# Kernel tuning notes

Hardware: AMD Instinct MI355X
Metric: run time of the kernel (lower is better)

Reference implementation:

```python
import jax, jax.numpy as jnp
import numpy as np

EMBED_DIM = 1024
NUM_HEADS = 16
HEAD_DIM = EMBED_DIM // NUM_HEADS


def setup_inputs() -> dict:
    key = jax.random.key(0)
    ks = jax.random.split(key, 8)
    B, S, D = 4, 2048, EMBED_DIM
    scale = 1.0 / np.sqrt(D)
    return {
        "values": jax.random.normal(ks[0], (B, S, D), jnp.float32),
        "keys": jax.random.normal(ks[1], (B, S, D), jnp.float32),
        "query": jax.random.normal(ks[2], (B, S, D), jnp.float32),
        "Wv": jax.random.normal(ks[3], (D, D), jnp.float32) * scale,
        "Wk": jax.random.normal(ks[4], (D, D), jnp.float32) * scale,
        "Wq": jax.random.normal(ks[5], (D, D), jnp.float32) * scale,
        "Wo": jax.random.normal(ks[6], (D, D), jnp.float32) * scale,
        "bo": jnp.zeros((D,), jnp.float32),
    }


def reference(values, keys, query, Wv, Wk, Wq, Wo, bo):
    N = query.shape[0]
    H, Dh = NUM_HEADS, HEAD_DIM
    # torch Linear: x @ W.T  (weights stored [out, in])
    v = (values @ Wv.T).reshape(N, -1, H, Dh)
    k = (keys @ Wk.T).reshape(N, -1, H, Dh)
    q = (query @ Wq.T).reshape(N, -1, H, Dh)
    # energy: [N, H, q, k]
    energy = jnp.einsum("nqhd,nkhd->nhqk", q, k)
    # NOTE: original scales by sqrt(embed_dim), not sqrt(head_dim)
    attn = jax.nn.softmax(energy / jnp.sqrt(jnp.float32(EMBED_DIM)), axis=3)
    out = jnp.einsum("nhql,nlhd->nqhd", attn, v).reshape(N, -1, H * Dh)
    return out @ Wo.T + bo
```

## Files before the change

### kernel.cpp

```cpp
#include <hip/hip_runtime.h>
#include <stdint.h>

#define S_LEN   2048
#define D_MODEL 1024
#define N_HEADS 16
#define D_HEAD  64
#define BATCH   4
#define GM      8192
#define GN      1024
#define GK      1024

typedef __attribute__((ext_vector_type(8)))  short short8;
typedef __attribute__((ext_vector_type(4)))  short short4v;
typedef __attribute__((ext_vector_type(4)))  float f32x4;
typedef __attribute__((ext_vector_type(16))) float f32x16;

__device__ __forceinline__ short f2bf(float f) {
  unsigned u = __builtin_bit_cast(unsigned, f);
  u += 0x7fffu + ((u >> 16) & 1u);
  return (short)(u >> 16);
}

__device__ __forceinline__ unsigned cvt_pk_bf16(float lo, float hi) {
  unsigned r;
  asm("v_cvt_pk_bf16_f32 %0, %1, %2" : "=v"(r) : "v"(lo), "v"(hi));
  return r;
}

__device__ __forceinline__ short8 cvtf8(const float4 f0, const float4 f1) {
  unsigned u[4] = { cvt_pk_bf16(f0.x, f0.y), cvt_pk_bf16(f0.z, f0.w),
                    cvt_pk_bf16(f1.x, f1.y), cvt_pk_bf16(f1.z, f1.w) };
  return __builtin_bit_cast(short8, *(ulonglong2*)u);
}

__device__ __forceinline__ void gload_lds16(const short* g, short* lds_base) {
  __builtin_amdgcn_global_load_lds(
      (const __attribute__((address_space(1))) void*)(const void*)g,
      (__attribute__((address_space(3))) void*)(void*)lds_base, 16, 0, 0);
}

__global__ __launch_bounds__(256)
void cast_w(const float* __restrict__ W0, const float* __restrict__ W1,
            const float* __restrict__ W2, const float* __restrict__ W3,
            short* __restrict__ O0, short* __restrict__ O1,
            short* __restrict__ O2, short* __restrict__ O3)
{
  const int y = blockIdx.y;
  const float* src = (y == 0) ? W0 : (y == 1) ? W1 : (y == 2) ? W2 : W3;
  short*       dst = (y == 0) ? O0 : (y == 1) ? O1 : (y == 2) ? O2 : O3;
  const int gid = blockIdx.x * 256 + threadIdx.x;
  const int row = gid >> 7, gr = gid & 127;
  const int og  = (gr & ~7) | ((gr & 7) ^ (row & 7));
  const float* p = src + row * 1024 + gr * 8;
  short8 v = cvtf8(*(const float4*)p, *(const float4*)(p + 4));
  *(short8*)(dst + row * 1024 + og * 8) = v;
}

__global__ __launch_bounds__(256, 3)
void gemm_qkv(const float* __restrict__ Aq, const float* __restrict__ Ak,
              const float* __restrict__ Av,
              const short* __restrict__ Bq, const short* __restrict__ Bk,
              const short* __restrict__ Bv,
              short* __restrict__ Cq, short* __restrict__ Ck,
              short* __restrict__ Cv, float qscale)
{
  __shared__ short As[128 * 64];
  __shared__ short Bs[128 * 64];

  const int p  = blockIdx.x + (blockIdx.y << 3) + (blockIdx.z << 9);
  const int lg = (p & 7) * 192 + (p >> 3);
  const int z  = lg >> 9;
  const int by = (lg >> 3) & 63;
  const int bx = lg & 7;

  const float* Af = (z == 0) ? Aq : (z == 1) ? Ak : Av;
  const short* Bw = (z == 0) ? Bq : (z == 1) ? Bk : Bv;

  const int t = threadIdx.x;
  const int l = t & 63, w = t >> 6;
  const int lo = l & 15, g = l >> 4;
  const int wr = (w >> 1) * 64, wc = (w & 1) * 64;

  const int srow0 = w * 8 + (l >> 3);
  const int sg = l & 7;

  f32x4 acc[4][4] = {};

  for (int kk = 0; kk < GK; kk += 64) {
#pragma unroll
    for (int i = 0; i < 4; ++i) {
      const int row = i * 32 + srow0;
      gload_lds16(Bw + (size_t)(bx * 128 + row) * GK + kk + sg * 8,
                  (short*)((char*)Bs + i * 4096 + w * 1024));
    }
#pragma unroll
    for (int i = 0; i < 4; ++i) {
      const int row = i * 32 + srow0;
      const float* p2 = Af + (size_t)(by * 128 + row) * GK + kk + sg * 8;
      short8 v = cvtf8(*(const float4*)p2, *(const float4*)(p2 + 4));
      *(short8*)(&As[row * 64 + ((sg ^ (row & 7)) * 8)]) = v;
    }
    __syncthreads();

#pragma unroll
    for (int kh = 0; kh < 2; ++kh) {
      short8 a[4], b[4];
      const int gg = ((kh * 4 + g) ^ (lo & 7)) * 8;
#pragma unroll
      for (int mi = 0; mi < 4; ++mi)
        a[mi] = *(const short8*)(&As[(wr + mi * 16 + lo) * 64 + gg]);
#pragma unroll
      for (int ni = 0; ni < 4; ++ni)
        b[ni] = *(const short8*)(&Bs[(wc + ni * 16 + lo) * 64 + gg]);
#pragma unroll
      for (int mi = 0; mi < 4; ++mi)
#pragma unroll
        for (int ni = 0; ni < 4; ++ni)
          acc[mi][ni] = __builtin_amdgcn_mfma_f32_16x16x32_bf16(a[mi], b[ni], acc[mi][ni], 0, 0, 0);
    }
    __syncthreads();
  }

  const int rbase = by * 128 + wr + g * 4;
  const int cbase = bx * 128 + wc + lo;

  if (z < 2) {
    short* C = (z == 0) ? Cq : Ck;
    const float scale = (z == 0) ? qscale : 1.0f;
#pragma unroll
    for (int mi = 0; mi < 4; ++mi)
#pragma unroll
      for (int ni = 0; ni < 4; ++ni)
#pragma unroll
        for (int r = 0; r < 4; ++r)
          C[(size_t)(rbase + mi * 16 + r) * GN + cbase + ni * 16] = f2bf(acc[mi][ni][r] * scale);
  } else {
#pragma unroll
    for (int mi = 0; mi < 4; ++mi)
#pragma unroll
      for (int ni = 0; ni < 4; ++ni) {
        short4v v = {f2bf(acc[mi][ni][0]), f2bf(acc[mi][ni][1]),
                     f2bf(acc[mi][ni][2]), f2bf(acc[mi][ni][3])};
        *(short4v*)(&Cv[(size_t)(cbase + ni * 16) * GM + rbase + mi * 16]) = v;
      }
  }
}

__global__ __launch_bounds__(256, 3)
void gemm_out(const short* __restrict__ Ab, const short* __restrict__ Bw,
              float* __restrict__ C, const float* __restrict__ bias)
{
  __shared__ short As[128 * 64];
  __shared__ short Bs[128 * 64];

  const int p  = blockIdx.x + (blockIdx.y << 3);
  const int lg = (p & 7) * 64 + (p >> 3);
  const int by = lg >> 3;
  const int bx = lg & 7;

  const int t = threadIdx.x;
  const int l = t & 63, w = t >> 6;
  const int lo = l & 15, g = l >> 4;
  const int wr = (w >> 1) * 64, wc = (w & 1) * 64;

  const int srow0 = w * 8 + (l >> 3);
  const int sg = l & 7;

  f32x4 acc[4][4] = {};

  for (int kk = 0; kk < GK; kk += 64) {
#pragma unroll
    for (int i = 0; i < 4; ++i) {
      const int row = i * 32 + srow0;
      gload_lds16(Bw + (size_t)(bx * 128 + row) * GK + kk + sg * 8,
                  (short*)((char*)Bs + i * 4096 + w * 1024));
      gload_lds16(Ab + (size_t)(by * 128 + row) * GK + kk + sg * 8,
                  (short*)((char*)As + i * 4096 + w * 1024));
    }
    __syncthreads();

#pragma unroll
    for (int kh = 0; kh < 2; ++kh) {
      short8 a[4], b[4];
      const int gg = ((kh * 4 + g) ^ (lo & 7)) * 8;
#pragma unroll
      for (int mi = 0; mi < 4; ++mi)
        a[mi] = *(const short8*)(&As[(wr + mi * 16 + lo) * 64 + gg]);
#pragma unroll
      for (int ni = 0; ni < 4; ++ni)
        b[ni] = *(const short8*)(&Bs[(wc + ni * 16 + lo) * 64 + gg]);
#pragma unroll
      for (int mi = 0; mi < 4; ++mi)
#pragma unroll
        for (int ni = 0; ni < 4; ++ni)
          acc[mi][ni] = __builtin_amdgcn_mfma_f32_16x16x32_bf16(a[mi], b[ni], acc[mi][ni], 0, 0, 0);
    }
    __syncthreads();
  }

  const int rbase = by * 128 + wr + g * 4;
  const int cbase = bx * 128 + wc + lo;
#pragma unroll
  for (int ni = 0; ni < 4; ++ni) {
    const float bs = bias[cbase + ni * 16];
#pragma unroll
    for (int mi = 0; mi < 4; ++mi)
#pragma unroll
      for (int r = 0; r < 4; ++r)
        C[(size_t)(rbase + mi * 16 + r) * GN + cbase + ni * 16] = acc[mi][ni][r] + bs;
  }
}

__global__ __launch_bounds__(256, 3)
void attn_fwd4(const short* __restrict__ Q, const short* __restrict__ Kp,
               const short* __restrict__ Vt, short* __restrict__ O)
{
  __shared__ __align__(16) char smem[32768];

  const int bid = blockIdx.x;
  const int ol = ((bid & 7) << 7) | (bid >> 3);
  const int qt = ol & 15, h = (ol >> 4) & 15, n = ol >> 8;

  const int t = threadIdx.x, w = t >> 6, l = t & 63;
  const int lq = l & 31, hi = l >> 5;

  const short* qp = Q + ((size_t)(n * S_LEN + qt * 128 + w * 32 + lq)) * D_MODEL
                      + h * D_HEAD + hi * 8;
  short8 qf[4];
#pragma unroll
  for (int kc = 0; kc < 4; ++kc) qf[kc] = *(const short8*)(qp + kc * 16);

  const int srow = (w * 2) * 8 + (l >> 3);
  const int sg0  = (l & 7) ^ (srow & 7);
  const short* kstage = Kp + ((size_t)(n * S_LEN + srow)) * D_MODEL + h * D_HEAD + sg0 * 8;
  const short* vstage = Vt + ((size_t)(h * D_HEAD + srow)) * GM + (size_t)n * S_LEN + sg0 * 8;

  const int woff = (w * 2) * 1024;

  gload_lds16(kstage,               (short*)(smem + woff));
  gload_lds16(kstage + 8 * D_MODEL, (short*)(smem + woff + 1024));
  gload_lds16(vstage,               (short*)(smem + 16384 + woff));
  gload_lds16(vstage + 8 * GM,      (short*)(smem + 16384 + woff + 1024));
  __syncthreads();

  f32x16 oacc[2] = {};
  float lsum = 0.f;

  int cur = 0;
  for (int it = 0; it < S_LEN / 64; ++it) {
    const char* Kc = smem + cur * 8192;
    const char* Vc = smem + 16384 + cur * 8192;

    if (it + 1 < S_LEN / 64) {
      const int kvn = (it + 1) * 64;
      const int nxt = (cur ^ 1) * 8192;
      gload_lds16(kstage + (size_t)kvn * D_MODEL,       (short*)(smem + nxt + woff));
      gload_lds16(kstage + (size_t)(kvn + 8) * D_MODEL, (short*)(smem + nxt + woff + 1024));
      gload_lds16(vstage + kvn,                         (short*)(smem + 16384 + nxt + woff));
      gload_lds16(vstage + 8 * GM + kvn,                (short*)(smem + 16384 + nxt + woff + 1024));
    }

    f32x16 s0 = {}, s1 = {};
    __builtin_amdgcn_s_setprio(1);
#pragma unroll
    for (int kc = 0; kc < 4; ++kc) {
      const int r0 = lq, r1 = 32 + lq;
      const short8 k0 = *(const short8*)(Kc + r0 * 128 + (((kc * 2 + hi) ^ (r0 & 7)) << 4));
      const short8 k1 = *(const short8*)(Kc + r1 * 128 + (((kc * 2 + hi) ^ (r1 & 7)) << 4));
      s0 = __builtin_amdgcn_mfma_f32_32x32x16_bf16(k0, qf[kc], s0, 0, 0, 0);
      s1 = __builtin_amdgcn_mfma_f32_32x32x16_bf16(k1, qf[kc], s1, 0, 0, 0);
    }
    __builtin_amdgcn_s_setprio(0);

    float ps0 = 0.f, ps1 = 0.f, ps2 = 0.f, ps3 = 0.f;
    unsigned pk[16];
#pragma unroll
    for (int j = 0; j < 8; ++j) {
      const float p0 = __builtin_amdgcn_exp2f(s0[2 * j]);
      const float p1 = __builtin_amdgcn_exp2f(s0[2 * j + 1]);
      ps0 += p0; ps1 += p1;
      pk[j] = cvt_pk_bf16(p0, p1);
    }
#pragma unroll
    for (int j = 0; j < 8; ++j) {
      const float p0 = __builtin_amdgcn_exp2f(s1[2 * j]);
      const float p1 = __builtin_amdgcn_exp2f(s1[2 * j + 1]);
      ps2 += p0; ps3 += p1;
      pk[8 + j] = cvt_pk_bf16(p0, p1);
    }
    float psum = (ps0 + ps1) + (ps2 + ps3);
    psum += __shfl_xor(psum, 32, 64);
    lsum += psum;

    short8 pf[4];
#pragma unroll
    for (int kb = 0; kb < 2; ++kb)
#pragma unroll
      for (int ksl = 0; ksl < 2; ++ksl) {
        unsigned A0 = pk[kb * 8 + 4 * ksl];
        unsigned A1 = pk[kb * 8 + 4 * ksl + 1];
        unsigned B0 = pk[kb * 8 + 4 * ksl + 2];
        unsigned B1 = pk[kb * 8 + 4 * ksl + 3];
        asm("v_permlane32_swap_b32 %0, %1" : "+v"(A0), "+v"(B0));
        asm("v_permlane32_swap_b32 %0, %1" : "+v"(A1), "+v"(B1));
        unsigned wds[4] = {A0, A1, B0, B1};
        pf[kb * 2 + ksl] = __builtin_bit_cast(short8, *(ulonglong2*)wds);
      }

    __builtin_amdgcn_s_setprio(1);
#pragma unroll
    for (int dc = 0; dc < 2; ++dc)
#pragma unroll
      for (int ks = 0; ks < 4; ++ks) {
        const int rv = dc * 32 + lq;
        const short8 vfr = *(const short8*)(Vc + rv * 128 + (((ks * 2 + hi) ^ (rv & 7)) << 4));
        oacc[dc] = __builtin_amdgcn_mfma_f32_32x32x16_bf16(vfr, pf[ks], oacc[dc], 0, 0, 0);
      }
    __builtin_amdgcn_s_setprio(0);

    __syncthreads();
    cur ^= 1;
  }

  short (*Os)[32][72] = (short (*)[32][72])&smem[0];
  const float inv = __builtin_amdgcn_rcpf(lsum);
#pragma unroll
  for (int dc = 0; dc < 2; ++dc)
#pragma unroll
    for (int g = 0; g < 4; ++g) {
      const int d = 32 * dc + 8 * g + 4 * hi;
      short4v v = {f2bf(oacc[dc][4 * g] * inv),     f2bf(oacc[dc][4 * g + 1] * inv),
                   f2bf(oacc[dc][4 * g + 2] * inv), f2bf(oacc[dc][4 * g + 3] * inv)};
      *(short4v*)(&Os[w][lq][d]) = v;
    }

  const int ql = l >> 1, half = l & 1;
  short* op = O + ((size_t)(n * S_LEN + qt * 128 + w * 32 + ql)) * D_MODEL + h * D_HEAD;
#pragma unroll
  for (int j = 0; j < 4; ++j) {
    const int pg = (half * 4 + j) ^ (ql & 7);
    *(short8*)(op + pg * 8) = *(const short8*)(&Os[w][ql][half * 32 + j * 8]);
  }
}

extern "C" void kernel_launch(void* const* d_in, const int* in_sizes, int n_in,
                              void* d_out, int out_size, void* d_ws, size_t ws_size,
                              hipStream_t stream) {
  const float* values = (const float*)d_in[0];
  const float* keys   = (const float*)d_in[1];
  const float* query  = (const float*)d_in[2];
  const float* Wv     = (const float*)d_in[3];
  const float* Wk     = (const float*)d_in[4];
  const float* Wq     = (const float*)d_in[5];
  const float* Wo     = (const float*)d_in[6];
  const float* bo     = (const float*)d_in[7];
  float* out = (float*)d_out;

  short* wv = (short*)d_ws;
  short* wk = wv + (size_t)1024 * 1024;
  short* wq = wk + (size_t)1024 * 1024;
  short* wo = wq + (size_t)1024 * 1024;
  short* qp = wo + (size_t)1024 * 1024;
  short* kp = qp + (size_t)GM * GN;
  short* vt = kp + (size_t)GM * GN;
  short* ao = vt + (size_t)GM * GN;

  dim3 bb(256);
  const float qscale = 0.03125f * 1.44269504089f;

  cast_w<<<dim3(512, 4), bb, 0, stream>>>(Wv, Wk, Wq, Wo, wv, wk, wq, wo);

  gemm_qkv<<<dim3(GN / 128, GM / 128, 3), bb, 0, stream>>>(
      query, keys, values, wq, wk, wv, qp, kp, vt, qscale);

  attn_fwd4<<<dim3(S_LEN / 128 * N_HEADS * BATCH), bb, 0, stream>>>(qp, kp, vt, ao);

  gemm_out<<<dim3(GN / 128, GM / 128), bb, 0, stream>>>(ao, wo, out, bo);
}
```

Before: 214.6 us.

## Double-buffer LDS tiles in QKV and output projection GEMMs

Both projection GEMMs now keep two LDS stages: the next K-tile is fetched, with global-to-LDS loads for B and register prefetch plus bf16 conversion for the fp32 A operand, while MFMAs run on the current tile. This removes one barrier per iteration and hides global load latency behind compute. LDS use per block doubles and launch bounds drop from 3 to 2 blocks per CU, so occupancy falls and register pressure rises from the prefetch registers.

```diff
diff --git a/kernel.cpp b/kernel.cpp
--- a/kernel.cpp
+++ b/kernel.cpp
@@ -56,7 +56,7 @@
   *(short8*)(dst + row * 1024 + og * 8) = v;
 }
 
-__global__ __launch_bounds__(256, 3)
+__global__ __launch_bounds__(256, 2)
 void gemm_qkv(const float* __restrict__ Aq, const float* __restrict__ Ak,
               const float* __restrict__ Av,
               const short* __restrict__ Bq, const short* __restrict__ Bk,
@@ -64,8 +64,8 @@
               short* __restrict__ Cq, short* __restrict__ Ck,
               short* __restrict__ Cv, float qscale)
 {
-  __shared__ short As[128 * 64];
-  __shared__ short Bs[128 * 64];
+  __shared__ short As[2 * 8192];
+  __shared__ short Bs[2 * 8192];
 
   const int p  = blockIdx.x + (blockIdx.y << 3) + (blockIdx.z << 9);
   const int lg = (p & 7) * 192 + (p >> 3);
@@ -85,22 +85,40 @@
   const int sg = l & 7;
 
   f32x4 acc[4][4] = {};
-
-  for (int kk = 0; kk < GK; kk += 64) {
-#pragma unroll
-    for (int i = 0; i < 4; ++i) {
-      const int row = i * 32 + srow0;
-      gload_lds16(Bw + (size_t)(bx * 128 + row) * GK + kk + sg * 8,
-                  (short*)((char*)Bs + i * 4096 + w * 1024));
-    }
-#pragma unroll
-    for (int i = 0; i < 4; ++i) {
-      const int row = i * 32 + srow0;
-      const float* p2 = Af + (size_t)(by * 128 + row) * GK + kk + sg * 8;
-      short8 v = cvtf8(*(const float4*)p2, *(const float4*)(p2 + 4));
-      *(short8*)(&As[row * 64 + ((sg ^ (row & 7)) * 8)]) = v;
-    }
-    __syncthreads();
+  float4 ar0[4], ar1[4];
+
+#pragma unroll
+  for (int i = 0; i < 4; ++i) {
+    const int row = i * 32 + srow0;
+    const float* pa = Af + (size_t)(by * 128 + row) * GK + sg * 8;
+    ar0[i] = *(const float4*)pa;
+    ar1[i] = *(const float4*)(pa + 4);
+    gload_lds16(Bw + (size_t)(bx * 128 + row) * GK + sg * 8,
+                (short*)((char*)Bs + i * 4096 + w * 1024));
+  }
+#pragma unroll
+  for (int i = 0; i < 4; ++i) {
+    const int row = i * 32 + srow0;
+    *(short8*)(&As[row * 64 + ((sg ^ (row & 7)) * 8)]) = cvtf8(ar0[i], ar1[i]);
+  }
+  __syncthreads();
+
+  for (int it = 0; it < GK / 64; ++it) {
+    const int cur = it & 1;
+    const int nxt = cur ^ 1;
+
+    if (it + 1 < GK / 64) {
+      const int kn = (it + 1) * 64;
+#pragma unroll
+      for (int i = 0; i < 4; ++i) {
+        const int row = i * 32 + srow0;
+        gload_lds16(Bw + (size_t)(bx * 128 + row) * GK + kn + sg * 8,
+                    (short*)((char*)Bs + nxt * 16384 + i * 4096 + w * 1024));
+        const float* pa = Af + (size_t)(by * 128 + row) * GK + kn + sg * 8;
+        ar0[i] = *(const float4*)pa;
+        ar1[i] = *(const float4*)(pa + 4);
+      }
+    }
 
 #pragma unroll
     for (int kh = 0; kh < 2; ++kh) {
@@ -108,15 +126,23 @@
       const int gg = ((kh * 4 + g) ^ (lo & 7)) * 8;
 #pragma unroll
       for (int mi = 0; mi < 4; ++mi)
-        a[mi] = *(const short8*)(&As[(wr + mi * 16 + lo) * 64 + gg]);
+        a[mi] = *(const short8*)(&As[cur * 8192 + (wr + mi * 16 + lo) * 64 + gg]);
 #pragma unroll
       for (int ni = 0; ni < 4; ++ni)
-        b[ni] = *(const short8*)(&Bs[(wc + ni * 16 + lo) * 64 + gg]);
+        b[ni] = *(const short8*)(&Bs[cur * 8192 + (wc + ni * 16 + lo) * 64 + gg]);
 #pragma unroll
       for (int mi = 0; mi < 4; ++mi)
 #pragma unroll
         for (int ni = 0; ni < 4; ++ni)
           acc[mi][ni] = __builtin_amdgcn_mfma_f32_16x16x32_bf16(a[mi], b[ni], acc[mi][ni], 0, 0, 0);
+    }
+
+    if (it + 1 < GK / 64) {
+#pragma unroll
+      for (int i = 0; i < 4; ++i) {
+        const int row = i * 32 + srow0;
+        *(short8*)(&As[nxt * 8192 + row * 64 + ((sg ^ (row & 7)) * 8)]) = cvtf8(ar0[i], ar1[i]);
+      }
     }
     __syncthreads();
   }
@@ -146,12 +172,12 @@
   }
 }
 
-__global__ __launch_bounds__(256, 3)
+__global__ __launch_bounds__(256, 2)
 void gemm_out(const short* __restrict__ Ab, const short* __restrict__ Bw,
               float* __restrict__ C, const float* __restrict__ bias)
 {
-  __shared__ short As[128 * 64];
-  __shared__ short Bs[128 * 64];
+  __shared__ short As[2 * 8192];
+  __shared__ short Bs[2 * 8192];
 
   const int p  = blockIdx.x + (blockIdx.y << 3);
   const int lg = (p & 7) * 64 + (p >> 3);
@@ -168,16 +194,31 @@
 
   f32x4 acc[4][4] = {};
 
-  for (int kk = 0; kk < GK; kk += 64) {
-#pragma unroll
-    for (int i = 0; i < 4; ++i) {
-      const int row = i * 32 + srow0;
-      gload_lds16(Bw + (size_t)(bx * 128 + row) * GK + kk + sg * 8,
-                  (short*)((char*)Bs + i * 4096 + w * 1024));
-      gload_lds16(Ab + (size_t)(by * 128 + row) * GK + kk + sg * 8,
-                  (short*)((char*)As + i * 4096 + w * 1024));
-    }
-    __syncthreads();
+#pragma unroll
+  for (int i = 0; i < 4; ++i) {
+    const int row = i * 32 + srow0;
+    gload_lds16(Bw + (size_t)(bx * 128 + row) * GK + sg * 8,
+                (short*)((char*)Bs + i * 4096 + w * 1024));
+    gload_lds16(Ab + (size_t)(by * 128 + row) * GK + sg * 8,
+                (short*)((char*)As + i * 4096 + w * 1024));
+  }
+  __syncthreads();
+
+  for (int it = 0; it < GK / 64; ++it) {
+    const int cur = it & 1;
+    const int nxt = cur ^ 1;
+
+    if (it + 1 < GK / 64) {
+      const int kn = (it + 1) * 64;
+#pragma unroll
+      for (int i = 0; i < 4; ++i) {
+        const int row = i * 32 + srow0;
+        gload_lds16(Bw + (size_t)(bx * 128 + row) * GK + kn + sg * 8,
+                    (short*)((char*)Bs + nxt * 16384 + i * 4096 + w * 1024));
+        gload_lds16(Ab + (size_t)(by * 128 + row) * GK + kn + sg * 8,
+                    (short*)((char*)As + nxt * 16384 + i * 4096 + w * 1024));
+      }
+    }
 
 #pragma unroll
     for (int kh = 0; kh < 2; ++kh) {
@@ -185,10 +226,10 @@
       const int gg = ((kh * 4 + g) ^ (lo & 7)) * 8;
 #pragma unroll
       for (int mi = 0; mi < 4; ++mi)
-        a[mi] = *(const short8*)(&As[(wr + mi * 16 + lo) * 64 + gg]);
+        a[mi] = *(const short8*)(&As[cur * 8192 + (wr + mi * 16 + lo) * 64 + gg]);
 #pragma unroll
       for (int ni = 0; ni < 4; ++ni)
-        b[ni] = *(const short8*)(&Bs[(wc + ni * 16 + lo) * 64 + gg]);
+        b[ni] = *(const short8*)(&Bs[cur * 8192 + (wc + ni * 16 + lo) * 64 + gg]);
 #pragma unroll
       for (int mi = 0; mi < 4; ++mi)
 #pragma unroll
```

Result: faster. 197.2 us (-8.1%).
